# Optimization experiments

Hardware: AMD Instinct MI355X
Metric: run time of the kernel (lower is better)

The kernel has to match this reference:

```python
import jax, jax.numpy as jnp
import numpy as np

DIM = 256
FFN_DIM = 512
NH = 8
EPS = 1e-5


def ln(x, g, b):
    m = x.mean(-1, keepdims=True)
    v = ((x - m) ** 2).mean(-1, keepdims=True)
    return (x - m) / jnp.sqrt(v + EPS) * g + b


def setup_inputs() -> dict:
    key = jax.random.key(0)
    ks = jax.random.split(key, 16)
    B, L, C, H, W = 16, 16384, DIM, 128, 128
    s = 0.02
    return {
        "query": jax.random.normal(ks[0], (B, 1, C), jnp.float32),
        "mem": jax.random.normal(ks[1], (B, L, C), jnp.float32),
        "ior_emb": jax.random.uniform(ks[2], (B, NH, H, W), jnp.float32),
        # input_proj: Linear(dim,dim) + ReLU + LayerNorm
        "W_ip": jax.random.normal(ks[3], (C, C), jnp.float32) * s,
        "b_ip": jnp.zeros((C,), jnp.float32),
        "g_ip": jnp.ones((C,), jnp.float32),
        "be_ip": jnp.zeros((C,), jnp.float32),
        # q / kv projections
        "W_q": jax.random.normal(ks[4], (C, C), jnp.float32) * s,
        "b_q": jnp.zeros((C,), jnp.float32),
        "W_kv": jax.random.normal(ks[5], (C, 2 * C), jnp.float32) * s,
        "b_kv": jnp.zeros((2 * C,), jnp.float32),
        # norm_q, norm_ffn
        "g_q": jnp.ones((C,), jnp.float32),
        "be_q": jnp.zeros((C,), jnp.float32),
        "g_f": jnp.ones((C,), jnp.float32),
        "be_f": jnp.zeros((C,), jnp.float32),
        # ffn (Mlp)
        "W1": jax.random.normal(ks[6], (C, FFN_DIM), jnp.float32) * s,
        "b1": jnp.zeros((FFN_DIM,), jnp.float32),
        "W2": jax.random.normal(ks[7], (FFN_DIM, C), jnp.float32) * s,
        "b2": jnp.zeros((C,), jnp.float32),
    }


def reference(query, mem, ior_emb, W_ip, b_ip, g_ip, be_ip, W_q, b_q, W_kv, b_kv,
              g_q, be_q, g_f, be_f, W1, b1, W2, b2):
    B, L, C = mem.shape
    nh = ior_emb.shape[1]
    hd = C // nh
    scale = hd ** -0.5
    # input_proj(mem): Linear -> ReLU -> LayerNorm
    m = ln(jax.nn.relu(mem @ W_ip + b_ip), g_ip, be_ip)  # [B,L,C]
    kv = m @ W_kv + b_kv
    k, v = kv[..., :C], kv[..., C:]
    q = ln(query, g_q, be_q) @ W_q + b_q  # [B,1,C]
    # per-head split along channel == reshape (..., nh, hd)
    qh = q.reshape(B, 1, nh, hd)
    kh = k.reshape(B, L, nh, hd)
    vh = v.reshape(B, L, nh, hd)
    ior = ior_emb.reshape(B, nh, 1, L)
    scores = jnp.einsum('bqhd,blhd->bhql', qh, kh) * scale * ior  # [B,nh,1,L]
    attn = jax.nn.softmax(scores, axis=-1)
    out = jnp.einsum('bhql,blhd->bqhd', attn, vh).reshape(B, 1, C)
    x = out + query
    h = ln(x, g_f, be_f)
    ffn = jax.nn.gelu(h @ W1 + b1, approximate=False) @ W2 + b2
    return x + ffn
```

## Files before the change

kernel.cpp:

```cpp
#include <hip/hip_runtime.h>
#include <math.h>

#define CDIM 256
#define LDIM 16384
#define NH 8
#define HD 32
#define FFN 512
#define EPS 1e-5f
#define SCALE 0.17677669529663687f

#define RB 32
#define CHUNKS (LDIM/RB)
#define LDA 264

typedef __attribute__((ext_vector_type(8))) short short8;
typedef __attribute__((ext_vector_type(4))) float f32x4;

__device__ inline unsigned short f2bf(float x) {
    unsigned int u = __float_as_uint(x);
    unsigned int lsb = (u >> 16) & 1u;
    u += 0x7fffu + lsb;
    return (unsigned short)(u >> 16);
}


__global__ __launch_bounds__(256) void prep_kernel(const float* __restrict__ Wip,
                                                   const float* __restrict__ Wkv,
                                                   unsigned short* __restrict__ w1,
                                                   unsigned short* __restrict__ wkv,
                                                   const float* __restrict__ query,
                                                   const float* __restrict__ Wq,
                                                   const float* __restrict__ bq,
                                                   const float* __restrict__ gq,
                                                   const float* __restrict__ beq,
                                                   float* __restrict__ qs) {
    if (blockIdx.x < 512) {
        int idx = blockIdx.x * 256 + threadIdx.x;
        if (idx < 65536) {
            int j = idx & 7, l = (idx >> 3) & 63, c = (idx >> 9) & 15, t = idx >> 13;
            int k = t * 32 + (l >> 4) * 8 + j;
            int col = c * 16 + (l & 15);
            w1[idx] = f2bf(Wip[k * CDIM + col]);
        }
        {
            int j = idx & 7, l = (idx >> 3) & 63, c = (idx >> 9) & 31, t = idx >> 14;
            int k = t * 32 + (l >> 4) * 8 + j;
            int col = c * 16 + (l & 15);
            wkv[idx] = f2bf(Wkv[k * 2 * CDIM + col]);
        }
    } else {
        int b = blockIdx.x - 512;
        int tid = threadIdx.x;
        int wave = tid >> 6, lane = tid & 63;
        __shared__ float sh[CDIM];
        __shared__ float red[8];

        float x = query[b * CDIM + tid];
        float s = x, sq = x * x;
#pragma unroll
        for (int m = 32; m >= 1; m >>= 1) { s += __shfl_xor(s, m, 64); sq += __shfl_xor(sq, m, 64); }
        if (lane == 0) { red[wave] = s; red[4 + wave] = sq; }
        __syncthreads();
        float ts = red[0] + red[1] + red[2] + red[3];
        float tq = red[4] + red[5] + red[6] + red[7];
        float mean = ts * (1.f / CDIM);
        float var = tq * (1.f / CDIM) - mean * mean;
        float rstd = rsqrtf(var + EPS);
        sh[tid] = (x - mean) * rstd * gq[tid] + beq[tid];
        __syncthreads();

        float acc = bq[tid];
        for (int k = 0; k < CDIM; ++k) acc = fmaf(sh[k], Wq[k * CDIM + tid], acc);
        qs[b * CDIM + tid] = acc * SCALE;
    }
}


__global__ __launch_bounds__(256, 3) void main_kernel(const float* __restrict__ mem,
                                                      const unsigned short* __restrict__ w1,
                                                      const unsigned short* __restrict__ wkv,
                                                      const float* __restrict__ bip,
                                                      const float* __restrict__ gip,
                                                      const float* __restrict__ beip,
                                                      const float* __restrict__ bkv,
                                                      const float* __restrict__ ior,
                                                      const float* __restrict__ qs,
                                                      float* __restrict__ partials) {
    int blk = blockIdx.x;
    int b = blk / CHUNKS;
    int chunk = blk % CHUNKS;
    int row0 = chunk * RB;
    int tid = threadIdx.x;
    int w = tid >> 6, l = tid & 63;
    int quad = l >> 4, lx = l & 15;

    __shared__ unsigned short bufA[RB * LDA];
    __shared__ float iorS[NH][RB];
    __shared__ float redS[4][RB];
    __shared__ float redQ[4][RB];
    __shared__ float stats[2][RB];

    {
        int h0 = tid >> 5, r0 = tid & 31;
        iorS[h0][r0] = ior[((size_t)(b * NH + h0)) * LDIM + row0 + r0];
    }
    {
        const float4* src = (const float4*)(mem + ((size_t)b * LDIM + row0) * CDIM);
#pragma unroll
        for (int it = 0; it < 8; ++it) {
            int i = tid + 256 * it;
            int r = i >> 6, c4 = i & 63;
            float4 v = src[i];
            ushort4 u;
            u.x = f2bf(v.x); u.y = f2bf(v.y); u.z = f2bf(v.z); u.w = f2bf(v.w);
            *(ushort4*)&bufA[r * LDA + c4 * 4] = u;
        }
    }
    __syncthreads();

    int col[4];
#pragma unroll
    for (int ci = 0; ci < 4; ++ci) col[ci] = (4 * w + ci) * 16 + lx;

    f32x4 acc[2][4];
#pragma unroll
    for (int rt = 0; rt < 2; ++rt)
#pragma unroll
        for (int ci = 0; ci < 4; ++ci) acc[rt][ci] = (f32x4){0.f, 0.f, 0.f, 0.f};
#pragma unroll
    for (int t = 0; t < 8; ++t) {
        short8 bfrag[4];
#pragma unroll
        for (int ci = 0; ci < 4; ++ci)
            bfrag[ci] = *(const short8*)(w1 + (((size_t)(t * 16 + 4 * w + ci)) * 64 + l) * 8);
        short8 afrag[2];
#pragma unroll
        for (int rt = 0; rt < 2; ++rt)
            afrag[rt] = *(const short8*)(bufA + (rt * 16 + lx) * LDA + t * 32 + quad * 8);
#pragma unroll
        for (int rt = 0; rt < 2; ++rt)
#pragma unroll
            for (int ci = 0; ci < 4; ++ci)
                acc[rt][ci] = __builtin_amdgcn_mfma_f32_16x16x32_bf16(afrag[rt], bfrag[ci], acc[rt][ci], 0, 0, 0);
    }

    float bb[4], gg[4], ee[4];
#pragma unroll
    for (int ci = 0; ci < 4; ++ci) { bb[ci] = bip[col[ci]]; gg[ci] = gip[col[ci]]; ee[ci] = beip[col[ci]]; }

#pragma unroll
    for (int rt = 0; rt < 2; ++rt) {
#pragma unroll
        for (int reg = 0; reg < 4; ++reg) {
#pragma unroll
            for (int ci = 0; ci < 4; ++ci)
                acc[rt][ci][reg] = fmaxf(acc[rt][ci][reg] + bb[ci], 0.f);
            float s = acc[rt][0][reg] + acc[rt][1][reg] + acc[rt][2][reg] + acc[rt][3][reg];
            float q = acc[rt][0][reg] * acc[rt][0][reg] + acc[rt][1][reg] * acc[rt][1][reg]
                    + acc[rt][2][reg] * acc[rt][2][reg] + acc[rt][3][reg] * acc[rt][3][reg];
#pragma unroll
            for (int m = 8; m >= 1; m >>= 1) { s += __shfl_xor(s, m, 64); q += __shfl_xor(q, m, 64); }
            if (lx == 0) {
                int row = rt * 16 + quad * 4 + reg;
                redS[w][row] = s;
                redQ[w][row] = q;
            }
        }
    }
    __syncthreads();
    if (tid < RB) {
        float s = redS[0][tid] + redS[1][tid] + redS[2][tid] + redS[3][tid];
        float q = redQ[0][tid] + redQ[1][tid] + redQ[2][tid] + redQ[3][tid];
        float mean = s * (1.f / CDIM);
        float var = q * (1.f / CDIM) - mean * mean;
        stats[0][tid] = mean;
        stats[1][tid] = rsqrtf(var + EPS);
    }
    __syncthreads();

#pragma unroll
    for (int rt = 0; rt < 2; ++rt)
#pragma unroll
        for (int reg = 0; reg < 4; ++reg) {
            int row = rt * 16 + quad * 4 + reg;
            float mean = stats[0][row], rstd = stats[1][row];
#pragma unroll
            for (int ci = 0; ci < 4; ++ci) {
                float y = (acc[rt][ci][reg] - mean) * rstd * gg[ci] + ee[ci];
                bufA[row * LDA + col[ci]] = f2bf(y);
            }
        }
    __syncthreads();

    f32x4 acc2[2][4], acc3[2][4];
#pragma unroll
    for (int rt = 0; rt < 2; ++rt)
#pragma unroll
        for (int ci = 0; ci < 4; ++ci) {
            acc2[rt][ci] = (f32x4){0.f, 0.f, 0.f, 0.f};
            acc3[rt][ci] = (f32x4){0.f, 0.f, 0.f, 0.f};
        }
#pragma unroll
    for (int t = 0; t < 8; ++t) {
        short8 bfragK[4], bfragV[4];
#pragma unroll
        for (int ci = 0; ci < 4; ++ci) {
            bfragK[ci] = *(const short8*)(wkv + (((size_t)(t * 32 + 4 * w + ci)) * 64 + l) * 8);
            bfragV[ci] = *(const short8*)(wkv + (((size_t)(t * 32 + 16 + 4 * w + ci)) * 64 + l) * 8);
        }
        short8 afrag[2];
#pragma unroll
        for (int rt = 0; rt < 2; ++rt)
            afrag[rt] = *(const short8*)(bufA + (rt * 16 + lx) * LDA + t * 32 + quad * 8);
#pragma unroll
        for (int rt = 0; rt < 2; ++rt)
#pragma unroll
            for (int ci = 0; ci < 4; ++ci) {
                acc2[rt][ci] = __builtin_amdgcn_mfma_f32_16x16x32_bf16(afrag[rt], bfragK[ci], acc2[rt][ci], 0, 0, 0);
                acc3[rt][ci] = __builtin_amdgcn_mfma_f32_16x16x32_bf16(afrag[rt], bfragV[ci], acc3[rt][ci], 0, 0, 0);
            }
    }

    float qv[4], bk[4];
#pragma unroll
    for (int ci = 0; ci < 4; ++ci) { qv[ci] = qs[b * CDIM + col[ci]]; bk[ci] = bkv[col[ci]]; }

    float p0[8], p1[8];
    float M0 = -1e30f, M1 = -1e30f;
#pragma unroll
    for (int rt = 0; rt < 2; ++rt)
#pragma unroll
        for (int reg = 0; reg < 4; ++reg) {
            float s0 = (acc2[rt][0][reg] + bk[0]) * qv[0] + (acc2[rt][1][reg] + bk[1]) * qv[1];
            float s1 = (acc2[rt][2][reg] + bk[2]) * qv[2] + (acc2[rt][3][reg] + bk[3]) * qv[3];
#pragma unroll
            for (int m = 8; m >= 1; m >>= 1) { s0 += __shfl_xor(s0, m, 64); s1 += __shfl_xor(s1, m, 64); }
            int row = rt * 16 + quad * 4 + reg;
            s0 *= iorS[2 * w][row];
            s1 *= iorS[2 * w + 1][row];
            p0[rt * 4 + reg] = s0;
            p1[rt * 4 + reg] = s1;
            M0 = fmaxf(M0, s0);
            M1 = fmaxf(M1, s1);
        }
    M0 = fmaxf(M0, __shfl_xor(M0, 16, 64)); M0 = fmaxf(M0, __shfl_xor(M0, 32, 64));
    M1 = fmaxf(M1, __shfl_xor(M1, 16, 64)); M1 = fmaxf(M1, __shfl_xor(M1, 32, 64));
    float S0 = 0.f, S1 = 0.f;
#pragma unroll
    for (int i = 0; i < 8; ++i) {
        p0[i] = __expf(p0[i] - M0); S0 += p0[i];
        p1[i] = __expf(p1[i] - M1); S1 += p1[i];
    }
    S0 += __shfl_xor(S0, 16, 64); S0 += __shfl_xor(S0, 32, 64);
    S1 += __shfl_xor(S1, 16, 64); S1 += __shfl_xor(S1, 32, 64);

    float o[4];
#pragma unroll
    for (int ci = 0; ci < 4; ++ci) {
        float bo = bkv[CDIM + col[ci]];
        const float* pp = (ci < 2) ? p0 : p1;
        float a = 0.f;
#pragma unroll
        for (int rt = 0; rt < 2; ++rt)
#pragma unroll
            for (int reg = 0; reg < 4; ++reg)
                a = fmaf(pp[rt * 4 + reg], acc3[rt][ci][reg] + bo, a);
        a += __shfl_xor(a, 16, 64);
        a += __shfl_xor(a, 32, 64);
        o[ci] = a;
    }

    float* P0 = &partials[((size_t)blk * NH + 2 * w) * 34];
    float* P1 = P0 + 34;
    if (quad == 0) {
        P0[2 + lx] = o[0];
        P0[2 + 16 + lx] = o[1];
        P1[2 + lx] = o[2];
        P1[2 + 16 + lx] = o[3];
        if (lx == 0) { P0[0] = M0; P0[1] = S0; P1[0] = M1; P1[1] = S1; }
    }
}


__global__ __launch_bounds__(64) void combine_kernel(const float* __restrict__ partials,
                                                     float* __restrict__ attnout) {
    int bh = blockIdx.x;
    int b = bh >> 3, h = bh & 7;
    int lane = threadIdx.x;

    float M = -1e30f;
    for (int c = lane; c < CHUNKS; c += 64)
        M = fmaxf(M, partials[(((size_t)b * CHUNKS + c) * NH + h) * 34]);
#pragma unroll
    for (int m = 32; m >= 1; m >>= 1) M = fmaxf(M, __shfl_xor(M, m, 64));

    float S = 0.f;
    for (int c = lane; c < CHUNKS; c += 64) {
        const float* P = &partials[(((size_t)b * CHUNKS + c) * NH + h) * 34];
        S += P[1] * __expf(P[0] - M);
    }
#pragma unroll
    for (int m = 32; m >= 1; m >>= 1) S += __shfl_xor(S, m, 64);

    int d = lane & 31, half = lane >> 5;
    float O = 0.f;
    for (int c = half; c < CHUNKS; c += 2) {
        const float* P = &partials[(((size_t)b * CHUNKS + c) * NH + h) * 34];
        O = fmaf(P[2 + d], __expf(P[0] - M), O);
    }
    O += __shfl_xor(O, 32, 64);
    if (lane < 32) attnout[b * CDIM + h * HD + d] = O / S;
}


__global__ __launch_bounds__(256) void epilogue_kernel(const float* __restrict__ attnout,
                                                       const float* __restrict__ query,
                                                       const float* __restrict__ gf,
                                                       const float* __restrict__ bef,
                                                       const float* __restrict__ W1,
                                                       const float* __restrict__ b1,
                                                       const float* __restrict__ W2,
                                                       const float* __restrict__ b2,
                                                       float* __restrict__ out) {
    int b = blockIdx.x;
    int tid = threadIdx.x;
    int wave = tid >> 6, lane = tid & 63;
    __shared__ float sh[FFN];
    __shared__ float red[8];

    float x = attnout[b * CDIM + tid] + query[b * CDIM + tid];
    float s = x, sq = x * x;
#pragma unroll
    for (int m = 32; m >= 1; m >>= 1) { s += __shfl_xor(s, m, 64); sq += __shfl_xor(sq, m, 64); }
    if (lane == 0) { red[wave] = s; red[4 + wave] = sq; }
    __syncthreads();
    float ts = red[0] + red[1] + red[2] + red[3];
    float tq = red[4] + red[5] + red[6] + red[7];
    float mean = ts * (1.f / CDIM);
    float var = tq * (1.f / CDIM) - mean * mean;
    float rstd = rsqrtf(var + EPS);
    sh[tid] = (x - mean) * rstd * gf[tid] + bef[tid];
    __syncthreads();

    float t[2];
#pragma unroll
    for (int i = 0; i < 2; ++i) {
        int f = tid + 256 * i;
        float a = b1[f];
        for (int k = 0; k < CDIM; ++k) a = fmaf(sh[k], W1[k * FFN + f], a);
        t[i] = 0.5f * a * (1.f + erff(a * 0.7071067811865476f));
    }
    __syncthreads();
    sh[tid] = t[0];
    sh[tid + 256] = t[1];
    __syncthreads();

    float y = b2[tid];
    for (int f = 0; f < FFN; ++f) y = fmaf(sh[f], W2[f * CDIM + tid], y);
    out[b * CDIM + tid] = x + y;
}


extern "C" void kernel_launch(void* const* d_in, const int* in_sizes, int n_in,
                              void* d_out, int out_size, void* d_ws, size_t ws_size,
                              hipStream_t stream) {
    const float* query = (const float*)d_in[0];
    const float* mem   = (const float*)d_in[1];
    const float* ior   = (const float*)d_in[2];
    const float* Wip   = (const float*)d_in[3];
    const float* bip   = (const float*)d_in[4];
    const float* gip   = (const float*)d_in[5];
    const float* beip  = (const float*)d_in[6];
    const float* Wq    = (const float*)d_in[7];
    const float* bq    = (const float*)d_in[8];
    const float* Wkv   = (const float*)d_in[9];
    const float* bkv   = (const float*)d_in[10];
    const float* gq    = (const float*)d_in[11];
    const float* beq   = (const float*)d_in[12];
    const float* gf    = (const float*)d_in[13];
    const float* bef   = (const float*)d_in[14];
    const float* W1    = (const float*)d_in[15];
    const float* b1    = (const float*)d_in[16];
    const float* W2    = (const float*)d_in[17];
    const float* b2    = (const float*)d_in[18];
    float* out = (float*)d_out;

    char* ws = (char*)d_ws;
    float* qs             = (float*)(ws);
    float* attnout        = (float*)(ws + 16384);
    float* partials       = (float*)(ws + 32768);
    unsigned short* w1sw  = (unsigned short*)(ws + 32768 + 8912896);
    unsigned short* wkvsw = (unsigned short*)(ws + 32768 + 8912896 + 131072);

    const int B = 16;

    prep_kernel<<<512 + B, 256, 0, stream>>>(Wip, Wkv, w1sw, wkvsw, query, Wq, bq, gq, beq, qs);
    main_kernel<<<B * CHUNKS, 256, 0, stream>>>(mem, w1sw, wkvsw, bip, gip, beip, bkv, ior, qs, partials);
    combine_kernel<<<B * NH, 64, 0, stream>>>(partials, attnout);
    epilogue_kernel<<<B, 256, 0, stream>>>(attnout, query, gf, bef, W1, b1, W2, b2, out);
}
```

Baseline: 616.0 us.

## Fuse softmax combine and FFN epilogue into one tail kernel; raise main occupancy

Merges the split-softmax combine kernel and the LayerNorm+FFN epilogue kernel into a single 512-thread-per-batch tail kernel. Each wave reduces one head's partials, the attention output stays in shared memory, and the FFN runs in the same block. This removes one launch and the global attnout round trip. It also raises main_kernel's launch_bounds min-blocks from 3 to 4, which may force register spilling. The tail now runs on only 16 blocks with 8 waves, which reduces combine parallelism compared with the earlier 128 blocks.

```diff
diff --git a/kernel.cpp b/kernel.cpp
--- a/kernel.cpp
+++ b/kernel.cpp
@@ -76,7 +76,7 @@
 }
 
 
-__global__ __launch_bounds__(256, 3) void main_kernel(const float* __restrict__ mem,
+__global__ __launch_bounds__(256, 4) void main_kernel(const float* __restrict__ mem,
                                                       const unsigned short* __restrict__ w1,
                                                       const unsigned short* __restrict__ wkv,
                                                       const float* __restrict__ bip,
@@ -282,21 +282,32 @@
 }
 
 
-__global__ __launch_bounds__(64) void combine_kernel(const float* __restrict__ partials,
-                                                     float* __restrict__ attnout) {
-    int bh = blockIdx.x;
-    int b = bh >> 3, h = bh & 7;
-    int lane = threadIdx.x;
-
+__global__ __launch_bounds__(512) void tail_kernel(const float* __restrict__ partials,
+                                                   const float* __restrict__ query,
+                                                   const float* __restrict__ gf,
+                                                   const float* __restrict__ bef,
+                                                   const float* __restrict__ W1,
+                                                   const float* __restrict__ b1,
+                                                   const float* __restrict__ W2,
+                                                   const float* __restrict__ b2,
+                                                   float* __restrict__ out) {
+    int b = blockIdx.x;
+    int tid = threadIdx.x;
+    int h = tid >> 6, lane = tid & 63;
+    __shared__ float xsh[CDIM];
+    __shared__ float sh2[FFN];
+    __shared__ float red[16];
+
+    const float* Pb = partials + (size_t)b * CHUNKS * NH * 34;
     float M = -1e30f;
     for (int c = lane; c < CHUNKS; c += 64)
-        M = fmaxf(M, partials[(((size_t)b * CHUNKS + c) * NH + h) * 34]);
+        M = fmaxf(M, Pb[((size_t)c * NH + h) * 34]);
 #pragma unroll
     for (int m = 32; m >= 1; m >>= 1) M = fmaxf(M, __shfl_xor(M, m, 64));
 
     float S = 0.f;
     for (int c = lane; c < CHUNKS; c += 64) {
-        const float* P = &partials[(((size_t)b * CHUNKS + c) * NH + h) * 34];
+        const float* P = &Pb[((size_t)c * NH + h) * 34];
         S += P[1] * __expf(P[0] - M);
     }
 #pragma unroll
@@ -305,59 +316,42 @@
     int d = lane & 31, half = lane >> 5;
     float O = 0.f;
     for (int c = half; c < CHUNKS; c += 2) {
-        const float* P = &partials[(((size_t)b * CHUNKS + c) * NH + h) * 34];
+        const float* P = &Pb[((size_t)c * NH + h) * 34];
         O = fmaf(P[2 + d], __expf(P[0] - M), O);
     }
     O += __shfl_xor(O, 32, 64);
-    if (lane < 32) attnout[b * CDIM + h * HD + d] = O / S;
-}
-
-
-__global__ __launch_bounds__(256) void epilogue_kernel(const float* __restrict__ attnout,
-                                                       const float* __restrict__ query,
-                                                       const float* __restrict__ gf,
-                                                       const float* __restrict__ bef,
-                                                       const float* __restrict__ W1,
-                                                       const float* __restrict__ b1,
-                                                       const float* __restrict__ W2,
-                                                       const float* __restrict__ b2,
-                                                       float* __restrict__ out) {
-    int b = blockIdx.x;
-    int tid = threadIdx.x;
-    int wave = tid >> 6, lane = tid & 63;
-    __shared__ float sh[FFN];
-    __shared__ float red[8];
-
-    float x = attnout[b * CDIM + tid] + query[b * CDIM + tid];
-    float s = x, sq = x * x;
-#pragma unroll
-    for (int m = 32; m >= 1; m >>= 1) { s += __shfl_xor(s, m, 64); sq += __shfl_xor(sq, m, 64); }
-    if (lane == 0) { red[wave] = s; red[4 + wave] = sq; }
+    if (lane < 32) xsh[h * HD + d] = O / S;
+    __syncthreads();
+
+    float x = 0.f;
+    if (tid < CDIM) {
+        x = xsh[tid] + query[b * CDIM + tid];
+        float s = x, sq = x * x;
+#pragma unroll
+        for (int m = 32; m >= 1; m >>= 1) { s += __shfl_xor(s, m, 64); sq += __shfl_xor(sq, m, 64); }
+        if (lane == 0) { red[h] = s; red[8 + h] = sq; }
+    }
     __syncthreads();
     float ts = red[0] + red[1] + red[2] + red[3];
-    float tq = red[4] + red[5] + red[6] + red[7];
+    float tq = red[8] + red[9] + red[10] + red[11];
     float mean = ts * (1.f / CDIM);
     float var = tq * (1.f / CDIM) - mean * mean;
     float rstd = rsqrtf(var + EPS);
-    sh[tid] = (x - mean) * rstd * gf[tid] + bef[tid];
-    __syncthreads();
-
-    float t[2];
-#pragma unroll
-    for (int i = 0; i < 2; ++i) {
-        int f = tid + 256 * i;
-        float a = b1[f];
-        for (int k = 0; k < CDIM; ++k) a = fmaf(sh[k], W1[k * FFN + f], a);
-        t[i] = 0.5f * a * (1.f + erff(a * 0.7071067811865476f));
-    }
-    __syncthreads();
-    sh[tid] = t[0];
-    sh[tid + 256] = t[1];
-    __syncthreads();
-
-    float y = b2[tid];
-    for (int f = 0; f < FFN; ++f) y = fmaf(sh[f], W2[f * CDIM + tid], y);
-    out[b * CDIM + tid] = x + y;
+    if (tid < CDIM) xsh[tid] = (x - mean) * rstd * gf[tid] + bef[tid];
+    __syncthreads();
+
+    {
+        float a = b1[tid];
+        for (int k = 0; k < CDIM; ++k) a = fmaf(xsh[k], W1[k * FFN + tid], a);
+        sh2[tid] = 0.5f * a * (1.f + erff(a * 0.7071067811865476f));
+    }
+    __syncthreads();
+
+    if (tid < CDIM) {
+        float y = b2[tid];
+        for (int f = 0; f < FFN; ++f) y = fmaf(sh2[f], W2[f * CDIM + tid], y);
+        out[b * CDIM + tid] = x + y;
+    }
 }
 
 
@@ -387,15 +381,13 @@
 
     char* ws = (char*)d_ws;
     float* qs             = (float*)(ws);
-    float* attnout        = (float*)(ws + 16384);
-    float* partials       = (float*)(ws + 32768);
-    unsigned short* w1sw  = (unsigned short*)(ws + 32768 + 8912896);
-    unsigned short* wkvsw = (unsigned short*)(ws + 32768 + 8912896 + 131072);
+    float* partials       = (float*)(ws + 16384);
+    unsigned short* w1sw  = (unsigned short*)(ws + 16384 + 8912896);
+    unsigned short* wkvsw = (unsigned short*)(ws + 16384 + 8912896 + 131072);
 
     const int B = 16;
 
     prep_kernel<<<512 + B, 256, 0, stream>>>(Wip, Wkv, w1sw, wkvsw, query, Wq, bq, gq, beq, qs);
     main_kernel<<<B * CHUNKS, 256, 0, stream>>>(mem, w1sw, wkvsw, bip, gip, beip, bkv, ior, qs, partials);
-    combine_kernel<<<B * NH, 64, 0, stream>>>(partials, attnout);
-    epilogue_kernel<<<B, 256, 0, stream>>>(attnout, query, gf, bef, W1, b1, W2, b2, out);
-}
+    tail_kernel<<<B, 512, 0, stream>>>(partials, query, gf, bef, W1, b1, W2, b2, out);
+}
```

Result: slower. 678.1 us (+10.1%).
